# Kernel optimization log

Measured on AMD Instinct MI355X. Metric: run time of the kernel, lower is better.

Reference implementation:

```python
import jax, jax.numpy as jnp
import numpy as np

SEQ, D_IN, D_OUT = 4096, 1024, 1024


def setup_inputs() -> dict:
    key = jax.random.key(0)
    kx, kq, kk, kv = jax.random.split(key, 4)
    x = jax.random.normal(kx, (SEQ, D_IN), dtype=jnp.float32)
    # original uses torch.rand (uniform [0,1)) for parameter init
    W_query = jax.random.uniform(kq, (D_IN, D_OUT), dtype=jnp.float32)
    W_key = jax.random.uniform(kk, (D_IN, D_OUT), dtype=jnp.float32)
    W_value = jax.random.uniform(kv, (D_IN, D_OUT), dtype=jnp.float32)
    return {"x": x, "W_query": W_query, "W_key": W_key, "W_value": W_value}


def reference(x, W_query, W_key, W_value):
    queries = x @ W_query          # [S, d_out]
    keys = x @ W_key               # [S, d_out]
    values = x @ W_value           # [S, d_out]
    scale = keys.shape[-1] ** 0.5
    attn_scores = queries @ keys.T # [S, S]
    attn_weights = jax.nn.softmax(attn_scores / scale, axis=-1)
    context_vec = attn_weights @ values  # [S, d_out]
    return context_vec
```

## Files before the change

kernel.cpp:

```cpp
#include <hip/hip_runtime.h>
#include <stdint.h>

#define SEQ 4096
#define DM 1024

typedef __attribute__((ext_vector_type(8))) short short8;
typedef __attribute__((ext_vector_type(4))) float f32x4;
typedef unsigned short ushort_t;

__device__ inline ushort_t f2bf(float f) {
  union { float f; uint32_t u; } v; v.f = f;
  return (ushort_t)((v.u + 0x7FFFu + ((v.u >> 16) & 1u)) >> 16);
}
__device__ inline float bf2f(ushort_t h) {
  union { uint32_t u; float f; } v; v.u = ((uint32_t)h) << 16;
  return v.f;
}

__device__ inline void async_copy16(const void* g, void* lds) {
  __builtin_amdgcn_global_load_lds(
      (const __attribute__((address_space(1))) uint32_t*)g,
      (__attribute__((address_space(3))) uint32_t*)lds, 16, 0, 0);
}


__global__ __launch_bounds__(256, 3)
void gemm_qkv(const ushort_t* __restrict__ A, const ushort_t* __restrict__ Bt,
              ushort_t* __restrict__ Qb, ushort_t* __restrict__ Kb,
              ushort_t* __restrict__ Vb) {
  __shared__ ushort_t As[2][128 * 32];
  __shared__ ushort_t Bs[2][128 * 32];
  const int t = threadIdx.x;
  const int wave = t >> 6, lane = t & 63;
  const int quad = lane >> 4, l16 = lane & 15;
  const int m0 = blockIdx.y * 128, n0 = blockIdx.x * 128;
  const bool is_v = (n0 >= 2048);
  const int wm = (wave & 1) * 64, wn = (wave >> 1) * 64;
  const int srow = lane >> 2;
  const int sf = (srow >> 1) & 3;
  const int gcol = (((lane & 3) - sf) & 3) * 8;
  const int rf = (l16 >> 1) & 3;
  const int aslot = ((quad + rf) & 3) * 8;

  f32x4 acc[4][4] = {};

  for (int k0 = 0; k0 < 1024; k0 += 32) {
#pragma unroll
    for (int i = 0; i < 2; ++i) {
      int c = wave * 2 + i;
      const ushort_t* ga = A + (size_t)(m0 + c * 16 + srow) * 2048 + k0 + gcol;
      const ushort_t* gb = Bt + (size_t)(n0 + c * 16 + srow) * 2048 + k0 + gcol;
      async_copy16(ga, As[0] + c * 512);
      async_copy16(gb, Bs[0] + c * 512);
      if (!is_v) {
        async_copy16(ga + 1024, As[1] + c * 512);
        async_copy16(gb + 1024, Bs[1] + c * 512);
      }
    }
    __syncthreads();
    short8 a[4], b[4], x[4];
#pragma unroll
    for (int i = 0; i < 4; ++i) {
      a[i] = *(const short8*)(As[0] + (wm + i * 16 + l16) * 32 + aslot);
      b[i] = *(const short8*)(Bs[0] + (wn + i * 16 + l16) * 32 + aslot);
    }
#pragma unroll
    for (int i = 0; i < 4; ++i)
#pragma unroll
      for (int j = 0; j < 4; ++j)
        acc[i][j] = __builtin_amdgcn_mfma_f32_16x16x32_bf16(a[i], b[j], acc[i][j], 0, 0, 0);
    if (!is_v) {
#pragma unroll
      for (int j = 0; j < 4; ++j)
        x[j] = *(const short8*)(Bs[1] + (wn + j * 16 + l16) * 32 + aslot);
#pragma unroll
      for (int i = 0; i < 4; ++i)
#pragma unroll
        for (int j = 0; j < 4; ++j)
          acc[i][j] = __builtin_amdgcn_mfma_f32_16x16x32_bf16(a[i], x[j], acc[i][j], 0, 0, 0);
#pragma unroll
      for (int i = 0; i < 4; ++i)
        x[i] = *(const short8*)(As[1] + (wm + i * 16 + l16) * 32 + aslot);
#pragma unroll
      for (int i = 0; i < 4; ++i)
#pragma unroll
        for (int j = 0; j < 4; ++j)
          acc[i][j] = __builtin_amdgcn_mfma_f32_16x16x32_bf16(x[i], b[j], acc[i][j], 0, 0, 0);
    }
    __syncthreads();
  }

  if (is_v) {
    const int cb = n0 - 2048;
#pragma unroll
    for (int i = 0; i < 4; ++i)
#pragma unroll
      for (int j = 0; j < 4; ++j)
#pragma unroll
        for (int r = 0; r < 4; ++r) {
          int row = m0 + wm + i * 16 + quad * 4 + r;
          int col = cb + wn + j * 16 + l16;
          Vb[(size_t)row * 1024 + col] = f2bf(acc[i][j][r]);
        }
  } else {
    ushort_t* Cm = (n0 < 1024) ? Qb : Kb;
    const int cb = n0 & 1023;
#pragma unroll
    for (int i = 0; i < 4; ++i)
#pragma unroll
      for (int j = 0; j < 4; ++j)
#pragma unroll
        for (int r = 0; r < 4; ++r) {
          int row = m0 + wm + i * 16 + quad * 4 + r;
          int col = cb + wn + j * 16 + l16;
          float v = acc[i][j][r];
          ushort_t h = f2bf(v);
          size_t base = (size_t)row * 2048 + col;
          Cm[base] = h;
          Cm[base + 1024] = f2bf(v - bf2f(h));
        }
  }
}

__global__ __launch_bounds__(256, 3)
void gemm_sc(const ushort_t* __restrict__ A, const ushort_t* __restrict__ Bt,
             float* __restrict__ C, float scale) {
  const int m0 = blockIdx.y * 128, n0 = blockIdx.x * 128;

  __shared__ ushort_t As[2][128 * 32];
  __shared__ ushort_t Bs[2][128 * 32];
  const int t = threadIdx.x;
  const int wave = t >> 6, lane = t & 63;
  const int quad = lane >> 4, l16 = lane & 15;
  const int wm = (wave & 1) * 64, wn = (wave >> 1) * 64;
  const int srow = lane >> 2;
  const int sf = (srow >> 1) & 3;
  const int gcol = (((lane & 3) - sf) & 3) * 8;
  const int rf = (l16 >> 1) & 3;
  const int aslot = ((quad + rf) & 3) * 8;

  f32x4 acc[4][4] = {};

  for (int k0 = 0; k0 < 1024; k0 += 32) {
#pragma unroll
    for (int i = 0; i < 2; ++i) {
      int c = wave * 2 + i;
      const ushort_t* ga = A + (size_t)(m0 + c * 16 + srow) * 2048 + k0 + gcol;
      const ushort_t* gb = Bt + (size_t)(n0 + c * 16 + srow) * 2048 + k0 + gcol;
      async_copy16(ga,        As[0] + c * 512);
      async_copy16(ga + 1024, As[1] + c * 512);
      async_copy16(gb,        Bs[0] + c * 512);
      async_copy16(gb + 1024, Bs[1] + c * 512);
    }
    __syncthreads();
    short8 a[4], b[4], x[4];
#pragma unroll
    for (int i = 0; i < 4; ++i) {
      a[i] = *(const short8*)(As[0] + (wm + i * 16 + l16) * 32 + aslot);
      b[i] = *(const short8*)(Bs[0] + (wn + i * 16 + l16) * 32 + aslot);
    }
#pragma unroll
    for (int i = 0; i < 4; ++i)
#pragma unroll
      for (int j = 0; j < 4; ++j)
        acc[i][j] = __builtin_amdgcn_mfma_f32_16x16x32_bf16(a[i], b[j], acc[i][j], 0, 0, 0);
#pragma unroll
    for (int j = 0; j < 4; ++j)
      x[j] = *(const short8*)(Bs[1] + (wn + j * 16 + l16) * 32 + aslot);
#pragma unroll
    for (int i = 0; i < 4; ++i)
#pragma unroll
      for (int j = 0; j < 4; ++j)
        acc[i][j] = __builtin_amdgcn_mfma_f32_16x16x32_bf16(a[i], x[j], acc[i][j], 0, 0, 0);
#pragma unroll
    for (int i = 0; i < 4; ++i)
      x[i] = *(const short8*)(As[1] + (wm + i * 16 + l16) * 32 + aslot);
#pragma unroll
    for (int i = 0; i < 4; ++i)
#pragma unroll
      for (int j = 0; j < 4; ++j)
        acc[i][j] = __builtin_amdgcn_mfma_f32_16x16x32_bf16(x[i], b[j], acc[i][j], 0, 0, 0);
    __syncthreads();
  }

#pragma unroll
  for (int i = 0; i < 4; ++i)
#pragma unroll
    for (int j = 0; j < 4; ++j)
#pragma unroll
      for (int r = 0; r < 4; ++r) {
        int row = m0 + wm + i * 16 + quad * 4 + r;
        int col = n0 + wn + j * 16 + l16;
        C[(size_t)row * SEQ + col] = acc[i][j][r] * scale;
      }
}

__global__ __launch_bounds__(256)
void gemm_pv(const ushort_t* __restrict__ P, const ushort_t* __restrict__ Vt,
             float* __restrict__ C) {
  const int id = blockIdx.x;
  const int g = ((id >> 6) << 3) | (id & 7);
  const int j = (id >> 3) & 7;
  const int z = g & 3, m = g >> 2;
  const int m0 = m * 128, n0 = j * 128, kbeg = z * 1024;

  __shared__ ushort_t As[128 * 64];
  __shared__ ushort_t Bs[128 * 64];
  const int t = threadIdx.x;
  const int wave = t >> 6, lane = t & 63;
  const int quad = lane >> 4, l16 = lane & 15;
  const int wm = (wave & 1) * 64, wn = (wave >> 1) * 64;
  const int srow = lane >> 3;
  const int gcol = (((lane & 7) - srow) & 7) * 8;
  const int rs = l16 & 7;

  f32x4 acc[4][4] = {};
  for (int k0 = kbeg; k0 < kbeg + 1024; k0 += 64) {
#pragma unroll
    for (int i = 0; i < 4; ++i) {
      int c = wave * 4 + i;
      async_copy16(P + (size_t)(m0 + c * 8 + srow) * 4096 + k0 + gcol,
                   As + c * 512);
      async_copy16(Vt + (size_t)(n0 + c * 8 + srow) * SEQ + k0 + gcol,
                   Bs + c * 512);
    }
    __syncthreads();
#pragma unroll
    for (int q = 0; q < 2; ++q) {
      short8 a[4], b[4];
#pragma unroll
      for (int i = 0; i < 4; ++i) {
        int slot = ((q * 4 + quad + rs) & 7) * 8;
        a[i] = *(const short8*)(As + (wm + i * 16 + l16) * 64 + slot);
        b[i] = *(const short8*)(Bs + (wn + i * 16 + l16) * 64 + slot);
      }
#pragma unroll
      for (int i = 0; i < 4; ++i)
#pragma unroll
        for (int j2 = 0; j2 < 4; ++j2)
          acc[i][j2] = __builtin_amdgcn_mfma_f32_16x16x32_bf16(a[i], b[j2], acc[i][j2], 0, 0, 0);
    }
    __syncthreads();
  }
#pragma unroll
  for (int i = 0; i < 4; ++i)
#pragma unroll
    for (int j2 = 0; j2 < 4; ++j2)
#pragma unroll
      for (int r = 0; r < 4; ++r) {
        int row = m0 + wm + i * 16 + quad * 4 + r;
        int col = n0 + wn + j2 * 16 + l16;
        atomicAdd(C + (size_t)row * DM + col, acc[i][j2][r]);
      }
}

__global__ __launch_bounds__(256)
void split_x(const float* __restrict__ x, ushort_t* __restrict__ Xp) {
  int idx = (blockIdx.x * 256 + threadIdx.x) * 4;
  int r = idx >> 10, c = idx & 1023;
  float4 v = *(const float4*)(x + idx);
  ushort4 hi, lo;
  hi.x = f2bf(v.x); lo.x = f2bf(v.x - bf2f(hi.x));
  hi.y = f2bf(v.y); lo.y = f2bf(v.y - bf2f(hi.y));
  hi.z = f2bf(v.z); lo.z = f2bf(v.z - bf2f(hi.z));
  hi.w = f2bf(v.w); lo.w = f2bf(v.w - bf2f(hi.w));
  *(ushort4*)(Xp + (size_t)r * 2048 + c) = hi;
  *(ushort4*)(Xp + (size_t)r * 2048 + 1024 + c) = lo;
}

__global__ __launch_bounds__(256)
void splitT_w3(const float* __restrict__ W0, const float* __restrict__ W1,
               const float* __restrict__ W2, ushort_t* __restrict__ Wp) {
  const float* W = (blockIdx.z == 0) ? W0 : (blockIdx.z == 1) ? W1 : W2;
  ushort_t* Wo = Wp + (size_t)blockIdx.z * DM * 2048;
  __shared__ float tile[64][65];
  const int bn = blockIdx.x * 64, bk = blockIdx.y * 64;
  const int tx = threadIdx.x & 63, ty = threadIdx.x >> 6;
#pragma unroll
  for (int i = ty; i < 64; i += 4)
    tile[i][tx] = W[(size_t)(bk + i) * DM + bn + tx];
  __syncthreads();
#pragma unroll
  for (int i = ty; i < 64; i += 4) {
    float v = tile[tx][i];
    ushort_t h = f2bf(v);
    Wo[(size_t)(bn + i) * 2048 + bk + tx] = h;
    Wo[(size_t)(bn + i) * 2048 + 1024 + bk + tx] = f2bf(v - bf2f(h));
  }
}

__global__ __launch_bounds__(256)
void transpose_bf16(const ushort_t* __restrict__ in, int istride,
                    ushort_t* __restrict__ out, int R) {
  __shared__ ushort_t tile[64][65];
  const int bc = blockIdx.x * 64, br = blockIdx.y * 64;
  const int tx = threadIdx.x & 63, ty = threadIdx.x >> 6;
#pragma unroll
  for (int i = ty; i < 64; i += 4)
    tile[i][tx] = in[(size_t)(br + i) * istride + bc + tx];
  __syncthreads();
#pragma unroll
  for (int i = ty; i < 64; i += 4)
    out[(size_t)(bc + i) * R + br + tx] = tile[tx][i];
}

__global__ __launch_bounds__(256)
void softmax_rows(const float* __restrict__ S, ushort_t* __restrict__ Pd) {
  const int row = blockIdx.x;
  const int t = threadIdx.x, lane = t & 63, wave = t >> 6;
  const float4* s4 = (const float4*)(S + (size_t)row * SEQ);
  float4 v[4];
  float m = -3.4e38f;
#pragma unroll
  for (int i = 0; i < 4; ++i) {
    v[i] = s4[i * 256 + t];
    m = fmaxf(m, fmaxf(fmaxf(v[i].x, v[i].y), fmaxf(v[i].z, v[i].w)));
  }
  __shared__ float redm[4], reds[4];
#pragma unroll
  for (int o = 32; o; o >>= 1) m = fmaxf(m, __shfl_xor(m, o));
  if (lane == 0) redm[wave] = m;
  __syncthreads();
  m = fmaxf(fmaxf(redm[0], redm[1]), fmaxf(redm[2], redm[3]));
  float sum = 0.f;
#pragma unroll
  for (int i = 0; i < 4; ++i) {
    v[i].x = __expf(v[i].x - m); v[i].y = __expf(v[i].y - m);
    v[i].z = __expf(v[i].z - m); v[i].w = __expf(v[i].w - m);
    sum += v[i].x + v[i].y + v[i].z + v[i].w;
  }
#pragma unroll
  for (int o = 32; o; o >>= 1) sum += __shfl_xor(sum, o);
  if (lane == 0) reds[wave] = sum;
  __syncthreads();
  const float inv = 1.f / (reds[0] + reds[1] + reds[2] + reds[3]);
  ushort4* p4 = (ushort4*)(Pd + (size_t)row * SEQ);
#pragma unroll
  for (int i = 0; i < 4; ++i) {
    ushort4 o;
    o.x = f2bf(v[i].x * inv); o.y = f2bf(v[i].y * inv);
    o.z = f2bf(v[i].z * inv); o.w = f2bf(v[i].w * inv);
    p4[i * 256 + t] = o;
  }
}

extern "C" void kernel_launch(void* const* d_in, const int* in_sizes, int n_in,
                              void* d_out, int out_size, void* d_ws, size_t ws_size,
                              hipStream_t stream) {
  const float* x  = (const float*)d_in[0];
  const float* Wq = (const float*)d_in[1];
  const float* Wk = (const float*)d_in[2];
  const float* Wv = (const float*)d_in[3];
  float* out = (float*)d_out;
  char* ws = (char*)d_ws;
  const size_t MB = (size_t)1 << 20;
  ushort_t* Xp   = (ushort_t*)(ws + 0 * MB);
  ushort_t* Wall = (ushort_t*)(ws + 16 * MB);
  ushort_t* Qb   = (ushort_t*)(ws + 28 * MB);
  ushort_t* Kb   = (ushort_t*)(ws + 44 * MB);
  ushort_t* Vb   = (ushort_t*)(ws + 60 * MB);
  ushort_t* VT   = (ushort_t*)(ws + 68 * MB);
  float*    S    = (float*)(ws + 76 * MB);
  ushort_t* Pd   = (ushort_t*)(ws + 0 * MB);

  hipMemsetAsync(d_out, 0, (size_t)SEQ * DM * sizeof(float), stream);

  split_x<<<SEQ * DM / 1024, 256, 0, stream>>>(x, Xp);
  splitT_w3<<<dim3(16, 16, 3), 256, 0, stream>>>(Wq, Wk, Wv, Wall);

  gemm_qkv<<<dim3(3 * DM / 128, SEQ / 128), 256, 0, stream>>>(
      Xp, Wall, Qb, Kb, Vb);

  transpose_bf16<<<dim3(DM / 64, SEQ / 64), 256, 0, stream>>>(Vb, 1024, VT, SEQ);

  gemm_sc<<<dim3(SEQ / 128, SEQ / 128), 256, 0, stream>>>(Qb, Kb, S, 0.03125f);

  softmax_rows<<<SEQ, 256, 0, stream>>>(S, Pd);

  gemm_pv<<<1024, 256, 0, stream>>>(Pd, VT, out);
}
```

Before: 344.1 us.

## Split V-projection into separate BK=64 path and use 32x32 MFMA in PV

The V tiles of the QKV GEMM now take an early-return branch with a 64-wide K tile and an 8-slot swizzle. This halves the number of K iterations and barriers for those blocks and removes the per-iteration is_v branches from the Q/K path. The PV GEMM switches from 16x16x32 to 32x32x16 bf16 MFMA with 2x2 accumulators of 16 floats each, which cuts the number of LDS fragment loads per MFMA flop. It also changes the output row mapping used by the atomic adds, which risks layout mistakes and different register pressure.

```diff
diff --git a/kernel.cpp b/kernel.cpp
--- a/kernel.cpp
+++ b/kernel.cpp
@@ -6,6 +6,7 @@
 
 typedef __attribute__((ext_vector_type(8))) short short8;
 typedef __attribute__((ext_vector_type(4))) float f32x4;
+typedef __attribute__((ext_vector_type(16))) float f32x16;
 typedef unsigned short ushort_t;
 
 __device__ inline ushort_t f2bf(float f) {
@@ -34,28 +35,73 @@
   const int wave = t >> 6, lane = t & 63;
   const int quad = lane >> 4, l16 = lane & 15;
   const int m0 = blockIdx.y * 128, n0 = blockIdx.x * 128;
-  const bool is_v = (n0 >= 2048);
   const int wm = (wave & 1) * 64, wn = (wave >> 1) * 64;
+
+  f32x4 acc[4][4] = {};
+
+  if (n0 >= 2048) {
+    ushort_t* Af = &As[0][0];
+    ushort_t* Bf = &Bs[0][0];
+    const int srow8 = lane >> 3;
+    const int gcol8 = (((lane & 7) - srow8) & 7) * 8;
+    const int rs = l16 & 7;
+    for (int k0 = 0; k0 < 1024; k0 += 64) {
+#pragma unroll
+      for (int i = 0; i < 4; ++i) {
+        int c = wave * 4 + i;
+        async_copy16(A + (size_t)(m0 + c * 8 + srow8) * 2048 + k0 + gcol8,
+                     Af + c * 512);
+        async_copy16(Bt + (size_t)(n0 + c * 8 + srow8) * 2048 + k0 + gcol8,
+                     Bf + c * 512);
+      }
+      __syncthreads();
+#pragma unroll
+      for (int q = 0; q < 2; ++q) {
+        short8 a[4], b[4];
+#pragma unroll
+        for (int i = 0; i < 4; ++i) {
+          int slot = ((q * 4 + quad + rs) & 7) * 8;
+          a[i] = *(const short8*)(Af + (wm + i * 16 + l16) * 64 + slot);
+          b[i] = *(const short8*)(Bf + (wn + i * 16 + l16) * 64 + slot);
+        }
+#pragma unroll
+        for (int i = 0; i < 4; ++i)
+#pragma unroll
+          for (int j = 0; j < 4; ++j)
+            acc[i][j] = __builtin_amdgcn_mfma_f32_16x16x32_bf16(a[i], b[j], acc[i][j], 0, 0, 0);
+      }
+      __syncthreads();
+    }
+    const int cb = n0 - 2048;
+#pragma unroll
+    for (int i = 0; i < 4; ++i)
+#pragma unroll
+      for (int j = 0; j < 4; ++j)
+#pragma unroll
+        for (int r = 0; r < 4; ++r) {
+          int row = m0 + wm + i * 16 + quad * 4 + r;
+          int col = cb + wn + j * 16 + l16;
+          Vb[(size_t)row * 1024 + col] = f2bf(acc[i][j][r]);
+        }
+    return;
+  }
+
   const int srow = lane >> 2;
   const int sf = (srow >> 1) & 3;
   const int gcol = (((lane & 3) - sf) & 3) * 8;
   const int rf = (l16 >> 1) & 3;
   const int aslot = ((quad + rf) & 3) * 8;
 
-  f32x4 acc[4][4] = {};
-
   for (int k0 = 0; k0 < 1024; k0 += 32) {
 #pragma unroll
     for (int i = 0; i < 2; ++i) {
       int c = wave * 2 + i;
       const ushort_t* ga = A + (size_t)(m0 + c * 16 + srow) * 2048 + k0 + gcol;
       const ushort_t* gb = Bt + (size_t)(n0 + c * 16 + srow) * 2048 + k0 + gcol;
-      async_copy16(ga, As[0] + c * 512);
-      async_copy16(gb, Bs[0] + c * 512);
-      if (!is_v) {
-        async_copy16(ga + 1024, As[1] + c * 512);
-        async_copy16(gb + 1024, Bs[1] + c * 512);
-      }
+      async_copy16(ga,        As[0] + c * 512);
+      async_copy16(ga + 1024, As[1] + c * 512);
+      async_copy16(gb,        Bs[0] + c * 512);
+      async_copy16(gb + 1024, Bs[1] + c * 512);
     }
     __syncthreads();
     short8 a[4], b[4], x[4];
@@ -69,57 +115,41 @@
 #pragma unroll
       for (int j = 0; j < 4; ++j)
         acc[i][j] = __builtin_amdgcn_mfma_f32_16x16x32_bf16(a[i], b[j], acc[i][j], 0, 0, 0);
-    if (!is_v) {
-#pragma unroll
-      for (int j = 0; j < 4; ++j)
-        x[j] = *(const short8*)(Bs[1] + (wn + j * 16 + l16) * 32 + aslot);
-#pragma unroll
-      for (int i = 0; i < 4; ++i)
-#pragma unroll
-        for (int j = 0; j < 4; ++j)
-          acc[i][j] = __builtin_amdgcn_mfma_f32_16x16x32_bf16(a[i], x[j], acc[i][j], 0, 0, 0);
-#pragma unroll
-      for (int i = 0; i < 4; ++i)
-        x[i] = *(const short8*)(As[1] + (wm + i * 16 + l16) * 32 + aslot);
-#pragma unroll
-      for (int i = 0; i < 4; ++i)
-#pragma unroll
-        for (int j = 0; j < 4; ++j)
-          acc[i][j] = __builtin_amdgcn_mfma_f32_16x16x32_bf16(x[i], b[j], acc[i][j], 0, 0, 0);
-    }
-    __syncthreads();
-  }
-
-  if (is_v) {
-    const int cb = n0 - 2048;
-#pragma unroll
-    for (int i = 0; i < 4; ++i)
-#pragma unroll
-      for (int j = 0; j < 4; ++j)
-#pragma unroll
-        for (int r = 0; r < 4; ++r) {
-          int row = m0 + wm + i * 16 + quad * 4 + r;
-          int col = cb + wn + j * 16 + l16;
-          Vb[(size_t)row * 1024 + col] = f2bf(acc[i][j][r]);
-        }
-  } else {
-    ushort_t* Cm = (n0 < 1024) ? Qb : Kb;
-    const int cb = n0 & 1023;
-#pragma unroll
-    for (int i = 0; i < 4; ++i)
-#pragma unroll
-      for (int j = 0; j < 4; ++j)
-#pragma unroll
-        for (int r = 0; r < 4; ++r) {
-          int row = m0 + wm + i * 16 + quad * 4 + r;
-          int col = cb + wn + j * 16 + l16;
-          float v = acc[i][j][r];
-          ushort_t h = f2bf(v);
-          size_t base = (size_t)row * 2048 + col;
-          Cm[base] = h;
-          Cm[base + 1024] = f2bf(v - bf2f(h));
-        }
-  }
+#pragma unroll
+    for (int j = 0; j < 4; ++j)
+      x[j] = *(const short8*)(Bs[1] + (wn + j * 16 + l16) * 32 + aslot);
+#pragma unroll
+    for (int i = 0; i < 4; ++i)
+#pragma unroll
+      for (int j = 0; j < 4; ++j)
+        acc[i][j] = __builtin_amdgcn_mfma_f32_16x16x32_bf16(a[i], x[j], acc[i][j], 0, 0, 0);
+#pragma unroll
+    for (int i = 0; i < 4; ++i)
+      x[i] = *(const short8*)(As[1] + (wm + i * 16 + l16) * 32 + aslot);
+#pragma unroll
+    for (int i = 0; i < 4; ++i)
+#pragma unroll
+      for (int j = 0; j < 4; ++j)
+        acc[i][j] = __builtin_amdgcn_mfma_f32_16x16x32_bf16(x[i], b[j], acc[i][j], 0, 0, 0);
+    __syncthreads();
+  }
+
+  ushort_t* Cm = (n0 < 1024) ? Qb : Kb;
+  const int cb = n0 & 1023;
+#pragma unroll
+  for (int i = 0; i < 4; ++i)
+#pragma unroll
+    for (int j = 0; j < 4; ++j)
+#pragma unroll
+      for (int r = 0; r < 4; ++r) {
+        int row = m0 + wm + i * 16 + quad * 4 + r;
+        int col = cb + wn + j * 16 + l16;
+        float v = acc[i][j][r];
+        ushort_t h = f2bf(v);
+        size_t base = (size_t)row * 2048 + col;
+        Cm[base] = h;
+        Cm[base + 1024] = f2bf(v - bf2f(h));
+      }
 }
 
 __global__ __launch_bounds__(256, 3)
@@ -200,21 +230,21 @@
              float* __restrict__ C) {
   const int id = blockIdx.x;
   const int g = ((id >> 6) << 3) | (id & 7);
-  const int j = (id >> 3) & 7;
+  const int jt = (id >> 3) & 7;
   const int z = g & 3, m = g >> 2;
-  const int m0 = m * 128, n0 = j * 128, kbeg = z * 1024;
+  const int m0 = m * 128, n0 = jt * 128, kbeg = z * 1024;
 
   __shared__ ushort_t As[128 * 64];
   __shared__ ushort_t Bs[128 * 64];
   const int t = threadIdx.x;
   const int wave = t >> 6, lane = t & 63;
-  const int quad = lane >> 4, l16 = lane & 15;
+  const int l32 = lane & 31, khalf = lane >> 5;
   const int wm = (wave & 1) * 64, wn = (wave >> 1) * 64;
   const int srow = lane >> 3;
   const int gcol = (((lane & 7) - srow) & 7) * 8;
-  const int rs = l16 & 7;
-
-  f32x4 acc[4][4] = {};
+  const int rrot = lane & 7;
+
+  f32x16 acc[2][2] = {};
   for (int k0 = kbeg; k0 < kbeg + 1024; k0 += 64) {
 #pragma unroll
     for (int i = 0; i < 4; ++i) {
@@ -226,31 +256,31 @@
     }
     __syncthreads();
 #pragma unroll
-    for (int q = 0; q < 2; ++q) {
-      short8 a[4], b[4];
-#pragma unroll
-      for (int i = 0; i < 4; ++i) {
-        int slot = ((q * 4 + quad + rs) & 7) * 8;
-        a[i] = *(const short8*)(As + (wm + i * 16 + l16) * 64 + slot);
-        b[i] = *(const short8*)(Bs + (wn + i * 16 + l16) * 64 + slot);
-      }
-#pragma unroll
-      for (int i = 0; i < 4; ++i)
-#pragma unroll
-        for (int j2 = 0; j2 < 4; ++j2)
-          acc[i][j2] = __builtin_amdgcn_mfma_f32_16x16x32_bf16(a[i], b[j2], acc[i][j2], 0, 0, 0);
-    }
-    __syncthreads();
-  }
-#pragma unroll
-  for (int i = 0; i < 4; ++i)
-#pragma unroll
-    for (int j2 = 0; j2 < 4; ++j2)
-#pragma unroll
-      for (int r = 0; r < 4; ++r) {
-        int row = m0 + wm + i * 16 + quad * 4 + r;
-        int col = n0 + wn + j2 * 16 + l16;
-        atomicAdd(C + (size_t)row * DM + col, acc[i][j2][r]);
+    for (int q = 0; q < 4; ++q) {
+      const int slot = ((q * 2 + khalf + rrot) & 7) * 8;
+      short8 a[2], b[2];
+#pragma unroll
+      for (int i = 0; i < 2; ++i) {
+        a[i] = *(const short8*)(As + (wm + i * 32 + l32) * 64 + slot);
+        b[i] = *(const short8*)(Bs + (wn + i * 32 + l32) * 64 + slot);
+      }
+#pragma unroll
+      for (int i = 0; i < 2; ++i)
+#pragma unroll
+        for (int j = 0; j < 2; ++j)
+          acc[i][j] = __builtin_amdgcn_mfma_f32_32x32x16_bf16(a[i], b[j], acc[i][j], 0, 0, 0);
+    }
+    __syncthreads();
+  }
+#pragma unroll
+  for (int i = 0; i < 2; ++i)
+#pragma unroll
+    for (int j = 0; j < 2; ++j)
+#pragma unroll
+      for (int r = 0; r < 16; ++r) {
+        int row = m0 + wm + i * 32 + (r & 3) + 8 * (r >> 2) + 4 * khalf;
+        int col = n0 + wn + j * 32 + l32;
+        atomicAdd(C + (size_t)row * DM + col, acc[i][j][r]);
       }
 }
 
```

Measured after the change: 340.3 us. About the same (-1.1%).
